# Kernel tuning notes

Hardware: AMD Instinct MI355X
Metric: run time of the kernel (lower is better)

The kernel has to match this reference:

```python
import jax, jax.numpy as jnp
import numpy as np

N = 100000
E = 800000
F_IN = 64
HID = 128


def setup_inputs() -> dict:
    key = jax.random.key(0)
    ks = jax.random.split(key, 10)
    x = jax.random.normal(ks[0], (N, F_IN), dtype=jnp.float32)
    edge_index = jax.random.randint(ks[1], (2, E), 0, N, dtype=jnp.int64)
    s = 0.05
    # PyG GraphConv: lin_rel (with bias) applied to aggregated neighbors, lin_root (no bias) to self
    return {
        "x": x,
        "edge_index": edge_index,
        "W1_rel": jax.random.normal(ks[2], (HID, F_IN), dtype=jnp.float32) * s,
        "b1": jnp.zeros((HID,), dtype=jnp.float32),
        "W1_root": jax.random.normal(ks[3], (HID, F_IN), dtype=jnp.float32) * s,
        "W2_rel": jax.random.normal(ks[4], (HID, HID), dtype=jnp.float32) * s,
        "b2": jnp.zeros((HID,), dtype=jnp.float32),
        "W2_root": jax.random.normal(ks[5], (HID, HID), dtype=jnp.float32) * s,
        "W_fc1": jax.random.normal(ks[6], (20, HID), dtype=jnp.float32) * s,
        "b_fc1": jnp.zeros((20,), dtype=jnp.float32),
        "W_fc2": jax.random.normal(ks[7], (1, 20), dtype=jnp.float32) * s,
        "b_fc2": jnp.zeros((1,), dtype=jnp.float32),
    }


def graph_conv(x, edge_index, W_rel, b_rel, W_root):
    # sum-aggregate source features onto destination nodes (PyG GraphConv, aggr='add')
    src, dst = edge_index[0], edge_index[1]
    agg = jax.ops.segment_sum(x[src], dst, num_segments=N)  # [N, F]
    return agg @ W_rel.T + b_rel + x @ W_root.T


def reference(x, edge_index, W1_rel, b1, W1_root, W2_rel, b2, W2_root,
              W_fc1, b_fc1, W_fc2, b_fc2):
    h = graph_conv(x, edge_index, W1_rel, b1, W1_root)
    h = jax.nn.elu(h)
    h = graph_conv(h, edge_index, W2_rel, b2, W2_root)
    h = jax.nn.relu(h @ W_fc1.T + b_fc1)
    out = h @ W_fc2.T + b_fc2  # [N, 1]
    return out
```

## Files before the change

kernel.cpp:

```cpp
#include <hip/hip_runtime.h>

#define N_NODES 100000
#define N_EDGES 800000
#define FIN 64
#define HID 128
#define NB1 391
#define SRCS_CAP (N_EDGES + 3 * N_NODES)
#define GI (1024 * 256)

typedef unsigned short ushort_t;
typedef __attribute__((ext_vector_type(8))) short short8;
typedef __attribute__((ext_vector_type(16))) float fx16;
typedef __attribute__((ext_vector_type(4))) unsigned short us4;

__device__ inline ushort_t f2bf(float f) {
    unsigned u = __float_as_uint(f);
    u += 0x7fffu + ((u >> 16) & 1u);
    return (ushort_t)(u >> 16);
}

__device__ inline void upadd(float* acc, uint4 A) {
    acc[0] += __uint_as_float(A.x << 16);
    acc[1] += __uint_as_float(A.x & 0xffff0000u);
    acc[2] += __uint_as_float(A.y << 16);
    acc[3] += __uint_as_float(A.y & 0xffff0000u);
    acc[4] += __uint_as_float(A.z << 16);
    acc[5] += __uint_as_float(A.z & 0xffff0000u);
    acc[6] += __uint_as_float(A.w << 16);
    acc[7] += __uint_as_float(A.w & 0xffff0000u);
}

__global__ __launch_bounds__(256) void init_kernel(
    const int* __restrict__ ei, const float* __restrict__ x,
    const float* __restrict__ W1rel, const float* __restrict__ W1root,
    const float* __restrict__ W2rel, const float* __restrict__ W2root,
    int* __restrict__ deg, int* __restrict__ flag, int* __restrict__ srcs,
    ushort_t* __restrict__ xb, ushort_t* __restrict__ h1b,
    ushort_t* __restrict__ Wb1, ushort_t* __restrict__ Wb2) {
    __shared__ int s[256];
    int t = threadIdx.x;
    int gtid = blockIdx.x * 256 + t;

    if (gtid < N_NODES) deg[gtid] = 0;
    for (int k = gtid; k < SRCS_CAP; k += GI) srcs[k] = N_NODES;
    for (int i = gtid; i < N_NODES * FIN / 4; i += GI) {
        float4 v = ((const float4*)x)[i];
        us4 o = {f2bf(v.x), f2bf(v.y), f2bf(v.z), f2bf(v.w)};
        ((us4*)xb)[i] = o;
    }
    us4 z = {0, 0, 0, 0};
    if (gtid < 16) ((us4*)xb)[(size_t)N_NODES * 16 + gtid] = z;
    if (gtid >= 16 && gtid < 48) ((us4*)h1b)[(size_t)N_NODES * 32 + (gtid - 16)] = z;
    if (gtid < HID * HID) {
        int n = gtid >> 7, k = gtid & 127;
        float v = (k < FIN) ? W1rel[n * FIN + k] : W1root[n * FIN + (k - FIN)];
        Wb1[gtid] = f2bf(v);
    }
    if (gtid < HID * 2 * HID) {
        int n = gtid >> 8, k = gtid & 255;
        float v = (k < HID) ? W2rel[n * HID + k] : W2root[n * HID + (k - HID)];
        Wb2[gtid] = f2bf(v);
    }
    if (blockIdx.x == 0) {
        int bad = 0;
        for (int i = t; i < 8192; i += 256) bad |= ei[2 * i + 1];
        s[t] = bad;
        __syncthreads();
        for (int d = 128; d > 0; d >>= 1) {
            if (t < d) s[t] |= s[t + d];
            __syncthreads();
        }
        if (t == 0) *flag = (s[0] != 0) ? 1 : 0;
    }
}

__global__ void hist_kernel(const int* __restrict__ w, const int* __restrict__ flag,
                            int* __restrict__ deg, int* __restrict__ rank) {
    int e = blockIdx.x * 256 + threadIdx.x;
    if (e >= N_EDGES) return;
    int is32 = *flag;
    int d = is32 ? w[N_EDGES + e] : w[2 * (N_EDGES + e)];
    rank[e] = atomicAdd(&deg[d], 1);
}

__global__ void scan1_kernel(const int* __restrict__ deg, int* __restrict__ off,
                             int* __restrict__ bsums) {
    __shared__ int s[256];
    int t = threadIdx.x;
    int i = blockIdx.x * 256 + t;
    int v = (i < N_NODES) ? ((deg[i] + 3) & ~3) : 0;
    s[t] = v;
    __syncthreads();
    for (int d = 1; d < 256; d <<= 1) {
        int w = (t >= d) ? s[t - d] : 0;
        __syncthreads();
        s[t] += w;
        __syncthreads();
    }
    if (i < N_NODES) off[i] = s[t] - v;
    if (t == 255) bsums[blockIdx.x] = s[255];
}

__global__ void scan23_kernel(int* __restrict__ off, const int* __restrict__ bsums) {
    __shared__ int s[256];
    int t = threadIdx.x, b = blockIdx.x;
    int pre = 0, tot = 0;
    for (int j = t; j < NB1; j += 256) {
        int v = bsums[j];
        if (j < b) pre += v;
        tot += v;
    }
    s[t] = pre;
    __syncthreads();
    for (int d = 128; d > 0; d >>= 1) {
        if (t < d) s[t] += s[t + d];
        __syncthreads();
    }
    int prefix = s[0];
    __syncthreads();
    int i = b * 256 + t;
    if (i < N_NODES) off[i] += prefix;
    if (b == 0) {
        s[t] = tot;
        __syncthreads();
        for (int d = 128; d > 0; d >>= 1) {
            if (t < d) s[t] += s[t + d];
            __syncthreads();
        }
        if (t == 0) off[N_NODES] = s[0];
    }
}

__global__ void scatter_kernel(const int* __restrict__ w, const int* __restrict__ flag,
                               const int* __restrict__ off, const int* __restrict__ rank,
                               int* __restrict__ srcs) {
    int e = blockIdx.x * 256 + threadIdx.x;
    if (e >= N_EDGES) return;
    int is32 = *flag;
    int s = is32 ? w[e] : w[2 * e];
    int d = is32 ? w[N_EDGES + e] : w[2 * (N_EDGES + e)];
    srcs[off[d] + rank[e]] = s;
}

__global__ void agg1_kernel(const ushort_t* __restrict__ xb, const int* __restrict__ off,
                            const int* __restrict__ srcs, ushort_t* __restrict__ aggb) {
    int wid = (blockIdx.x * 256 + threadIdx.x) >> 6;
    int lane = threadIdx.x & 63;
    int n = lane >> 3;
    unsigned c = lane & 7;
    int node = wid * 8 + n;
    int b = off[node], e = off[node + 1];
    float acc[8];
#pragma unroll
    for (int j = 0; j < 8; j++) acc[j] = 0.f;
    const uint4* rows = (const uint4*)xb;
    for (int p = b; p < e; p += 4) {
        int4 s = *(const int4*)(srcs + p);
        uint4 A = rows[(unsigned)s.x * 8u + c];
        uint4 B = rows[(unsigned)s.y * 8u + c];
        uint4 C = rows[(unsigned)s.z * 8u + c];
        uint4 D = rows[(unsigned)s.w * 8u + c];
        upadd(acc, A);
        upadd(acc, B);
        upadd(acc, C);
        upadd(acc, D);
    }
    uint4 o = {(unsigned)f2bf(acc[0]) | ((unsigned)f2bf(acc[1]) << 16),
               (unsigned)f2bf(acc[2]) | ((unsigned)f2bf(acc[3]) << 16),
               (unsigned)f2bf(acc[4]) | ((unsigned)f2bf(acc[5]) << 16),
               (unsigned)f2bf(acc[6]) | ((unsigned)f2bf(acc[7]) << 16)};
    ((uint4*)(aggb + (size_t)node * FIN))[c] = o;
}

__global__ void agg2_kernel(const ushort_t* __restrict__ h1b, const int* __restrict__ off,
                            const int* __restrict__ srcs, ushort_t* __restrict__ aggb) {
    int wid = (blockIdx.x * 256 + threadIdx.x) >> 6;
    int lane = threadIdx.x & 63;
    int n = lane >> 4;
    unsigned c = lane & 15;
    int node = wid * 4 + n;
    int b = off[node], e = off[node + 1];
    float acc[8];
#pragma unroll
    for (int j = 0; j < 8; j++) acc[j] = 0.f;
    const uint4* rows = (const uint4*)h1b;
    for (int p = b; p < e; p += 4) {
        int4 s = *(const int4*)(srcs + p);
        uint4 A = rows[(unsigned)s.x * 16u + c];
        uint4 B = rows[(unsigned)s.y * 16u + c];
        uint4 C = rows[(unsigned)s.z * 16u + c];
        uint4 D = rows[(unsigned)s.w * 16u + c];
        upadd(acc, A);
        upadd(acc, B);
        upadd(acc, C);
        upadd(acc, D);
    }
    uint4 o = {(unsigned)f2bf(acc[0]) | ((unsigned)f2bf(acc[1]) << 16),
               (unsigned)f2bf(acc[2]) | ((unsigned)f2bf(acc[3]) << 16),
               (unsigned)f2bf(acc[4]) | ((unsigned)f2bf(acc[5]) << 16),
               (unsigned)f2bf(acc[6]) | ((unsigned)f2bf(acc[7]) << 16)};
    ((uint4*)(aggb + (size_t)node * HID))[c] = o;
}

__global__ __launch_bounds__(256) void g1_kernel(
    const ushort_t* __restrict__ aggb, const ushort_t* __restrict__ xb,
    const ushort_t* __restrict__ Wb1, const float* __restrict__ b1,
    ushort_t* __restrict__ h1b) {
    __shared__ short8 wl8[2048];
    ushort_t* wl = (ushort_t*)wl8;
#pragma unroll
    for (int it = 0; it < 8; it++) {
        int q = it * 256 + threadIdx.x;
        int n = q >> 4, c = q & 15;
        short8 v = ((const short8*)Wb1)[q];
        *(short8*)(wl + n * HID + ((c ^ (n & 7)) << 3)) = v;
    }
    __syncthreads();

    int wave = threadIdx.x >> 6;
    int lane = threadIdx.x & 63;
    int nb = blockIdx.x * 128 + wave * 32;
    if (nb >= N_NODES) return;
    int half = lane >> 5, col = lane & 31;
    int nA = nb + col;
    if (nA >= N_NODES) nA = N_NODES - 1;

    short8 areg[8];
#pragma unroll
    for (int s = 0; s < 4; s++)
        areg[s] = *(const short8*)(aggb + (size_t)nA * FIN + s * 16 + half * 8);
#pragma unroll
    for (int s = 4; s < 8; s++)
        areg[s] = *(const short8*)(xb + (size_t)nA * FIN + (s - 4) * 16 + half * 8);

    fx16 acc[4];
#pragma unroll
    for (int jt = 0; jt < 4; jt++)
#pragma unroll
        for (int r = 0; r < 16; r++) acc[jt][r] = 0.f;

#pragma unroll
    for (int s = 0; s < 8; s++) {
        int c = 2 * s + half;
#pragma unroll
        for (int jt = 0; jt < 4; jt++) {
            int n = jt * 32 + col;
            short8 bq = *(const short8*)(wl + n * HID + ((c ^ (n & 7)) << 3));
            acc[jt] = __builtin_amdgcn_mfma_f32_32x32x16_bf16(areg[s], bq, acc[jt], 0, 0, 0);
        }
    }
#pragma unroll
    for (int jt = 0; jt < 4; jt++) {
        int j = jt * 32 + col;
        float bias = b1[j];
#pragma unroll
        for (int r = 0; r < 16; r++) {
            int node = nb + (r & 3) + 8 * (r >> 2) + 4 * half;
            if (node < N_NODES) {
                float v = acc[jt][r] + bias;
                v = v > 0.f ? v : __expf(v) - 1.f;
                h1b[(size_t)node * HID + j] = f2bf(v);
            }
        }
    }
}

__global__ __launch_bounds__(256) void g2h_kernel(
    const ushort_t* __restrict__ agg2b, const ushort_t* __restrict__ h1b,
    const ushort_t* __restrict__ Wb2, const float* __restrict__ b2,
    const float* __restrict__ Wfc1, const float* __restrict__ bfc1,
    const float* __restrict__ Wfc2, const float* __restrict__ bfc2,
    float* __restrict__ out) {
    __shared__ ushort_t smem[21504];
    ushort_t* wl = smem;
    ushort_t* wf = smem + 17408;

#pragma unroll
    for (int it = 0; it < 16; it++) {
        int idx = it * 256 + threadIdx.x;
        int m = idx >> 7, k = idx & 127;
        float v = (m < 20) ? Wfc1[m * HID + k] : 0.f;
        wf[m * 128 + (((k >> 3) ^ (m & 7)) << 3) + (k & 7)] = f2bf(v);
    }
#pragma unroll
    for (int it = 0; it < 8; it++) {
        int q = it * 256 + threadIdx.x;
        int n = q >> 4, c = q & 15;
        short8 v = *(const short8*)(Wb2 + (size_t)n * 256 + c * 8);
        *(short8*)(wl + n * 128 + ((c ^ (n & 7)) << 3)) = v;
    }

    int wave = threadIdx.x >> 6;
    int lane = threadIdx.x & 63;
    int half = lane >> 5, col = lane & 31;
    int nb = blockIdx.x * 128 + wave * 32;
    int nA = nb + col;
    if (nA >= N_NODES) nA = N_NODES - 1;

    short8 areg[16];
#pragma unroll
    for (int s = 0; s < 8; s++)
        areg[s] = *(const short8*)(agg2b + (size_t)nA * HID + s * 16 + half * 8);
#pragma unroll
    for (int s = 8; s < 16; s++)
        areg[s] = *(const short8*)(h1b + (size_t)nA * HID + (s - 8) * 16 + half * 8);

    fx16 acc[4];
#pragma unroll
    for (int jt = 0; jt < 4; jt++)
#pragma unroll
        for (int r = 0; r < 16; r++) acc[jt][r] = 0.f;

    __syncthreads();
#pragma unroll
    for (int s = 0; s < 8; s++) {
        int c = 2 * s + half;
#pragma unroll
        for (int jt = 0; jt < 4; jt++) {
            int n = jt * 32 + col;
            short8 bq = *(const short8*)(wl + n * 128 + ((c ^ (n & 7)) << 3));
            acc[jt] = __builtin_amdgcn_mfma_f32_32x32x16_bf16(areg[s], bq, acc[jt], 0, 0, 0);
        }
    }
    __syncthreads();
#pragma unroll
    for (int it = 0; it < 8; it++) {
        int q = it * 256 + threadIdx.x;
        int n = q >> 4, c = q & 15;
        short8 v = *(const short8*)(Wb2 + (size_t)n * 256 + 128 + c * 8);
        *(short8*)(wl + n * 128 + ((c ^ (n & 7)) << 3)) = v;
    }
    __syncthreads();
#pragma unroll
    for (int s = 8; s < 16; s++) {
        int c = 2 * (s - 8) + half;
#pragma unroll
        for (int jt = 0; jt < 4; jt++) {
            int n = jt * 32 + col;
            short8 bq = *(const short8*)(wl + n * 128 + ((c ^ (n & 7)) << 3));
            acc[jt] = __builtin_amdgcn_mfma_f32_32x32x16_bf16(areg[s], bq, acc[jt], 0, 0, 0);
        }
    }
    __syncthreads();

    ushort_t* tl = smem;
#pragma unroll
    for (int jt = 0; jt < 4; jt++) {
        int j = jt * 32 + col;
        float bias = b2[j];
#pragma unroll
        for (int r = 0; r < 16; r++) {
            int nl = wave * 32 + (r & 3) + 8 * (r >> 2) + 4 * half;
            tl[nl * 136 + j] = f2bf(acc[jt][r] + bias);
        }
    }
    __syncthreads();

    short8 af[8];
#pragma unroll
    for (int s = 0; s < 8; s++)
        af[s] = *(const short8*)(tl + (wave * 32 + col) * 136 + s * 16 + half * 8);
    fx16 fa;
#pragma unroll
    for (int r = 0; r < 16; r++) fa[r] = 0.f;
#pragma unroll
    for (int s = 0; s < 8; s++) {
        int c = 2 * s + half;
        short8 bw = *(const short8*)(wf + col * 128 + ((c ^ (col & 7)) << 3));
        fa = __builtin_amdgcn_mfma_f32_32x32x16_bf16(af[s], bw, fa, 0, 0, 0);
    }
    float biasv = (col < 20) ? bfc1[col] : 0.f;
    float w2v = (col < 20) ? Wfc2[col] : 0.f;
    float bz = bfc2[0];
    float red[16];
#pragma unroll
    for (int r = 0; r < 16; r++) {
        float v = fa[r] + biasv;
        v = (v > 0.f ? v : 0.f) * w2v;
        v += __shfl_xor(v, 1);
        v += __shfl_xor(v, 2);
        v += __shfl_xor(v, 4);
        v += __shfl_xor(v, 8);
        v += __shfl_xor(v, 16);
        red[r] = v;
    }
    if (col == 0) {
#pragma unroll
        for (int r = 0; r < 16; r++) {
            int nl = wave * 32 + (r & 3) + 8 * (r >> 2) + 4 * half;
            int ng = blockIdx.x * 128 + nl;
            if (ng < N_NODES) out[ng] = red[r] + bz;
        }
    }
}

extern "C" void kernel_launch(void* const* d_in, const int* in_sizes, int n_in,
                              void* d_out, int out_size, void* d_ws, size_t ws_size,
                              hipStream_t stream) {
    const float* x = (const float*)d_in[0];
    const int* ei = (const int*)d_in[1];
    const float* W1rel = (const float*)d_in[2];
    const float* b1 = (const float*)d_in[3];
    const float* W1root = (const float*)d_in[4];
    const float* W2rel = (const float*)d_in[5];
    const float* b2 = (const float*)d_in[6];
    const float* W2root = (const float*)d_in[7];
    const float* Wfc1 = (const float*)d_in[8];
    const float* bfc1 = (const float*)d_in[9];
    const float* Wfc2 = (const float*)d_in[10];
    const float* bfc2 = (const float*)d_in[11];
    float* out = (float*)d_out;

    char* ws = (char*)d_ws;
    size_t o = 0;
    auto alloc = [&](size_t bytes) {
        char* p = ws + o;
        o += (bytes + 255) & ~(size_t)255;
        return p;
    };
    int* deg = (int*)alloc((size_t)N_NODES * 4);
    int* off = (int*)alloc((size_t)(N_NODES + 1) * 4);
    int* bsums = (int*)alloc(4096);
    int* flag = (int*)alloc(256);
    int* rank = (int*)alloc((size_t)N_EDGES * 4);
    int* srcs = (int*)alloc((size_t)SRCS_CAP * 4);
    ushort_t* xb = (ushort_t*)alloc((size_t)(N_NODES + 1) * FIN * 2);
    ushort_t* agg1b = (ushort_t*)alloc((size_t)N_NODES * FIN * 2);
    ushort_t* h1b = (ushort_t*)alloc((size_t)(N_NODES + 1) * HID * 2);
    ushort_t* agg2b = (ushort_t*)alloc((size_t)N_NODES * HID * 2);
    ushort_t* Wb1 = (ushort_t*)alloc((size_t)HID * HID * 2);
    ushort_t* Wb2 = (ushort_t*)alloc((size_t)HID * 2 * HID * 2);

    const int GW = (N_NODES + 127) / 128;
    const int GA1 = N_NODES / 32;
    const int GA2 = N_NODES / 16;

    init_kernel<<<1024, 256, 0, stream>>>(ei, x, W1rel, W1root, W2rel, W2root,
                                          deg, flag, srcs, xb, h1b, Wb1, Wb2);
    hist_kernel<<<(N_EDGES + 255) / 256, 256, 0, stream>>>(ei, flag, deg, rank);
    scan1_kernel<<<NB1, 256, 0, stream>>>(deg, off, bsums);
    scan23_kernel<<<NB1, 256, 0, stream>>>(off, bsums);
    scatter_kernel<<<(N_EDGES + 255) / 256, 256, 0, stream>>>(ei, flag, off, rank, srcs);
    agg1_kernel<<<GA1, 256, 0, stream>>>(xb, off, srcs, agg1b);
    g1_kernel<<<GW, 256, 0, stream>>>(agg1b, xb, Wb1, b1, h1b);
    agg2_kernel<<<GA2, 256, 0, stream>>>(h1b, off, srcs, agg2b);
    g2h_kernel<<<GW, 256, 0, stream>>>(agg2b, h1b, Wb2, b2, Wfc1, bfc1, Wfc2, bfc2, out);
}
```

Baseline: 249.8 us.

## Fold layer-2 weights into fc1 and aggregate projected 20-dim features

```diff
diff --git a/kernel.cpp b/kernel.cpp
--- a/kernel.cpp
+++ b/kernel.cpp
@@ -34,9 +34,11 @@
     const int* __restrict__ ei, const float* __restrict__ x,
     const float* __restrict__ W1rel, const float* __restrict__ W1root,
     const float* __restrict__ W2rel, const float* __restrict__ W2root,
+    const float* __restrict__ b2, const float* __restrict__ Wfc1,
+    const float* __restrict__ bfc1, const float* __restrict__ Wfc2,
     int* __restrict__ deg, int* __restrict__ flag, int* __restrict__ srcs,
-    ushort_t* __restrict__ xb, ushort_t* __restrict__ h1b,
-    ushort_t* __restrict__ Wb1, ushort_t* __restrict__ Wb2) {
+    ushort_t* __restrict__ xb, ushort_t* __restrict__ Wb1,
+    ushort_t* __restrict__ Mb, float* __restrict__ cbp, float* __restrict__ w2p) {
     __shared__ int s[256];
     int t = threadIdx.x;
     int gtid = blockIdx.x * 256 + t;
@@ -50,18 +52,34 @@
     }
     us4 z = {0, 0, 0, 0};
     if (gtid < 16) ((us4*)xb)[(size_t)N_NODES * 16 + gtid] = z;
-    if (gtid >= 16 && gtid < 48) ((us4*)h1b)[(size_t)N_NODES * 32 + (gtid - 16)] = z;
     if (gtid < HID * HID) {
         int n = gtid >> 7, k = gtid & 127;
         float v = (k < FIN) ? W1rel[n * FIN + k] : W1root[n * FIN + (k - FIN)];
         Wb1[gtid] = f2bf(v);
     }
-    if (gtid < HID * 2 * HID) {
-        int n = gtid >> 8, k = gtid & 255;
-        float v = (k < HID) ? W2rel[n * HID + k] : W2root[n * HID + (k - HID)];
-        Wb2[gtid] = f2bf(v);
-    }
-    if (blockIdx.x == 0) {
+    if (blockIdx.x < 32) {
+        int idx = blockIdx.x * 256 + t;
+        int n = idx >> 7, k = idx & 127;
+        float acc = 0.f;
+        if (n < 20) {
+            for (int j = 0; j < HID; j++) acc += Wfc1[n * HID + j] * W2rel[j * HID + k];
+        } else if (n >= 32 && n < 52) {
+            int m = n - 32;
+            for (int j = 0; j < HID; j++) acc += Wfc1[m * HID + j] * W2root[j * HID + k];
+        }
+        Mb[idx] = f2bf(acc);
+    }
+    if (blockIdx.x == 32 && t < 32) {
+        float cv = 0.f, wv = 0.f;
+        if (t < 20) {
+            for (int j = 0; j < HID; j++) cv += Wfc1[t * HID + j] * b2[j];
+            cv += bfc1[t];
+            wv = Wfc2[t];
+        }
+        cbp[t] = cv;
+        w2p[t] = wv;
+    }
+    if (blockIdx.x == 33) {
         int bad = 0;
         for (int i = t; i < 8192; i += 256) bad |= ei[2 * i + 1];
         s[t] = bad;
@@ -172,36 +190,6 @@
     ((uint4*)(aggb + (size_t)node * FIN))[c] = o;
 }
 
-__global__ void agg2_kernel(const ushort_t* __restrict__ h1b, const int* __restrict__ off,
-                            const int* __restrict__ srcs, ushort_t* __restrict__ aggb) {
-    int wid = (blockIdx.x * 256 + threadIdx.x) >> 6;
-    int lane = threadIdx.x & 63;
-    int n = lane >> 4;
-    unsigned c = lane & 15;
-    int node = wid * 4 + n;
-    int b = off[node], e = off[node + 1];
-    float acc[8];
-#pragma unroll
-    for (int j = 0; j < 8; j++) acc[j] = 0.f;
-    const uint4* rows = (const uint4*)h1b;
-    for (int p = b; p < e; p += 4) {
-        int4 s = *(const int4*)(srcs + p);
-        uint4 A = rows[(unsigned)s.x * 16u + c];
-        uint4 B = rows[(unsigned)s.y * 16u + c];
-        uint4 C = rows[(unsigned)s.z * 16u + c];
-        uint4 D = rows[(unsigned)s.w * 16u + c];
-        upadd(acc, A);
-        upadd(acc, B);
-        upadd(acc, C);
-        upadd(acc, D);
-    }
-    uint4 o = {(unsigned)f2bf(acc[0]) | ((unsigned)f2bf(acc[1]) << 16),
-               (unsigned)f2bf(acc[2]) | ((unsigned)f2bf(acc[3]) << 16),
-               (unsigned)f2bf(acc[4]) | ((unsigned)f2bf(acc[5]) << 16),
-               (unsigned)f2bf(acc[6]) | ((unsigned)f2bf(acc[7]) << 16)};
-    ((uint4*)(aggb + (size_t)node * HID))[c] = o;
-}
-
 __global__ __launch_bounds__(256) void g1_kernel(
     const ushort_t* __restrict__ aggb, const ushort_t* __restrict__ xb,
     const ushort_t* __restrict__ Wb1, const float* __restrict__ b1,
@@ -265,133 +253,115 @@
     }
 }
 
-__global__ __launch_bounds__(256) void g2h_kernel(
-    const ushort_t* __restrict__ agg2b, const ushort_t* __restrict__ h1b,
-    const ushort_t* __restrict__ Wb2, const float* __restrict__ b2,
-    const float* __restrict__ Wfc1, const float* __restrict__ bfc1,
-    const float* __restrict__ Wfc2, const float* __restrict__ bfc2,
-    float* __restrict__ out) {
-    __shared__ ushort_t smem[21504];
-    ushort_t* wl = smem;
-    ushort_t* wf = smem + 17408;
-
-#pragma unroll
-    for (int it = 0; it < 16; it++) {
-        int idx = it * 256 + threadIdx.x;
-        int m = idx >> 7, k = idx & 127;
-        float v = (m < 20) ? Wfc1[m * HID + k] : 0.f;
-        wf[m * 128 + (((k >> 3) ^ (m & 7)) << 3) + (k & 7)] = f2bf(v);
-    }
-#pragma unroll
-    for (int it = 0; it < 8; it++) {
+__global__ __launch_bounds__(256) void g2_kernel(
+    const ushort_t* __restrict__ h1b, const ushort_t* __restrict__ Mb,
+    ushort_t* __restrict__ uvb) {
+    __shared__ short8 ml8[1024];
+    ushort_t* ml = (ushort_t*)ml8;
+    us4 z = {0, 0, 0, 0};
+    if (blockIdx.x == 0 && threadIdx.x < 8)
+        ((us4*)(uvb + (size_t)N_NODES * 64))[threadIdx.x] = z;
+#pragma unroll
+    for (int it = 0; it < 4; it++) {
         int q = it * 256 + threadIdx.x;
         int n = q >> 4, c = q & 15;
-        short8 v = *(const short8*)(Wb2 + (size_t)n * 256 + c * 8);
-        *(short8*)(wl + n * 128 + ((c ^ (n & 7)) << 3)) = v;
-    }
+        short8 v = ((const short8*)Mb)[q];
+        *(short8*)(ml + n * HID + ((c ^ (n & 7)) << 3)) = v;
+    }
+    __syncthreads();
 
     int wave = threadIdx.x >> 6;
     int lane = threadIdx.x & 63;
+    int nb = blockIdx.x * 128 + wave * 32;
+    if (nb >= N_NODES) return;
     int half = lane >> 5, col = lane & 31;
-    int nb = blockIdx.x * 128 + wave * 32;
     int nA = nb + col;
     if (nA >= N_NODES) nA = N_NODES - 1;
 
-    short8 areg[16];
+    short8 areg[8];
 #pragma unroll
     for (int s = 0; s < 8; s++)
-        areg[s] = *(const short8*)(agg2b + (size_t)nA * HID + s * 16 + half * 8);
-#pragma unroll
-    for (int s = 8; s < 16; s++)
-        areg[s] = *(const short8*)(h1b + (size_t)nA * HID + (s - 8) * 16 + half * 8);
-
-    fx16 acc[4];
-#pragma unroll
-    for (int jt = 0; jt < 4; jt++)
+        areg[s] = *(const short8*)(h1b + (size_t)nA * HID + s * 16 + half * 8);
+
+    fx16 acc[2];
+#pragma unroll
+    for (int jt = 0; jt < 2; jt++)
 #pragma unroll
         for (int r = 0; r < 16; r++) acc[jt][r] = 0.f;
 
-    __syncthreads();
 #pragma unroll
     for (int s = 0; s < 8; s++) {
         int c = 2 * s + half;
 #pragma unroll
-        for (int jt = 0; jt < 4; jt++) {
+        for (int jt = 0; jt < 2; jt++) {
             int n = jt * 32 + col;
-            short8 bq = *(const short8*)(wl + n * 128 + ((c ^ (n & 7)) << 3));
+            short8 bq = *(const short8*)(ml + n * HID + ((c ^ (n & 7)) << 3));
             acc[jt] = __builtin_amdgcn_mfma_f32_32x32x16_bf16(areg[s], bq, acc[jt], 0, 0, 0);
         }
     }
-    __syncthreads();
-#pragma unroll
-    for (int it = 0; it < 8; it++) {
-        int q = it * 256 + threadIdx.x;
-        int n = q >> 4, c = q & 15;
-        short8 v = *(const short8*)(Wb2 + (size_t)n * 256 + 128 + c * 8);
-        *(short8*)(wl + n * 128 + ((c ^ (n & 7)) << 3)) = v;
-    }
-    __syncthreads();
-#pragma unroll
-    for (int s = 8; s < 16; s++) {
-        int c = 2 * (s - 8) + half;
-#pragma unroll
-        for (int jt = 0; jt < 4; jt++) {
-            int n = jt * 32 + col;
-            short8 bq = *(const short8*)(wl + n * 128 + ((c ^ (n & 7)) << 3));
-            acc[jt] = __builtin_amdgcn_mfma_f32_32x32x16_bf16(areg[s], bq, acc[jt], 0, 0, 0);
-        }
-    }
-    __syncthreads();
-
-    ushort_t* tl = smem;
-#pragma unroll
-    for (int jt = 0; jt < 4; jt++) {
+#pragma unroll
+    for (int jt = 0; jt < 2; jt++) {
         int j = jt * 32 + col;
-        float bias = b2[j];
 #pragma unroll
         for (int r = 0; r < 16; r++) {
-            int nl = wave * 32 + (r & 3) + 8 * (r >> 2) + 4 * half;
-            tl[nl * 136 + j] = f2bf(acc[jt][r] + bias);
-        }
-    }
-    __syncthreads();
-
-    short8 af[8];
-#pragma unroll
-    for (int s = 0; s < 8; s++)
-        af[s] = *(const short8*)(tl + (wave * 32 + col) * 136 + s * 16 + half * 8);
-    fx16 fa;
-#pragma unroll
-    for (int r = 0; r < 16; r++) fa[r] = 0.f;
-#pragma unroll
-    for (int s = 0; s < 8; s++) {
-        int c = 2 * s + half;
-        short8 bw = *(const short8*)(wf + col * 128 + ((c ^ (col & 7)) << 3));
-        fa = __builtin_amdgcn_mfma_f32_32x32x16_bf16(af[s], bw, fa, 0, 0, 0);
-    }
-    float biasv = (col < 20) ? bfc1[col] : 0.f;
-    float w2v = (col < 20) ? Wfc2[col] : 0.f;
-    float bz = bfc2[0];
-    float red[16];
-#pragma unroll
-    for (int r = 0; r < 16; r++) {
-        float v = fa[r] + biasv;
-        v = (v > 0.f ? v : 0.f) * w2v;
-        v += __shfl_xor(v, 1);
-        v += __shfl_xor(v, 2);
-        v += __shfl_xor(v, 4);
-        v += __shfl_xor(v, 8);
-        v += __shfl_xor(v, 16);
-        red[r] = v;
-    }
-    if (col == 0) {
-#pragma unroll
-        for (int r = 0; r < 16; r++) {
-            int nl = wave * 32 + (r & 3) + 8 * (r >> 2) + 4 * half;
-            int ng = blockIdx.x * 128 + nl;
-            if (ng < N_NODES) out[ng] = red[r] + bz;
-        }
-    }
+            int node = nb + (r & 3) + 8 * (r >> 2) + 4 * half;
+            if (node < N_NODES) uvb[(size_t)node * 64 + j] = f2bf(acc[jt][r]);
+        }
+    }
+}
+
+__global__ void agg3h_kernel(const ushort_t* __restrict__ uvb, const int* __restrict__ off,
+                             const int* __restrict__ srcs, const float* __restrict__ cbp,
+                             const float* __restrict__ w2p, const float* __restrict__ bfc2,
+                             float* __restrict__ out) {
+    int wid = (blockIdx.x * 256 + threadIdx.x) >> 6;
+    int lane = threadIdx.x & 63;
+    int n = lane >> 2;
+    unsigned c = lane & 3;
+    int node0 = wid * 16 + n;
+    int node = (node0 < N_NODES) ? node0 : N_NODES - 1;
+    int b = off[node], e = off[node + 1];
+    float acc[8];
+#pragma unroll
+    for (int j = 0; j < 8; j++) acc[j] = 0.f;
+    const uint4* rows = (const uint4*)uvb;
+    for (int p = b; p < e; p += 4) {
+        int4 s = *(const int4*)(srcs + p);
+        uint4 A = rows[(unsigned)s.x * 8u + c];
+        uint4 B = rows[(unsigned)s.y * 8u + c];
+        uint4 C = rows[(unsigned)s.z * 8u + c];
+        uint4 D = rows[(unsigned)s.w * 8u + c];
+        upadd(acc, A);
+        upadd(acc, B);
+        upadd(acc, C);
+        upadd(acc, D);
+    }
+    uint4 V = rows[(size_t)node * 8u + 4u + c];
+    float vv[8];
+    vv[0] = __uint_as_float(V.x << 16);
+    vv[1] = __uint_as_float(V.x & 0xffff0000u);
+    vv[2] = __uint_as_float(V.y << 16);
+    vv[3] = __uint_as_float(V.y & 0xffff0000u);
+    vv[4] = __uint_as_float(V.z << 16);
+    vv[5] = __uint_as_float(V.z & 0xffff0000u);
+    vv[6] = __uint_as_float(V.w << 16);
+    vv[7] = __uint_as_float(V.w & 0xffff0000u);
+    float4 cba = ((const float4*)cbp)[c * 2];
+    float4 cbb = ((const float4*)cbp)[c * 2 + 1];
+    float4 w2a = ((const float4*)w2p)[c * 2];
+    float4 w2b = ((const float4*)w2p)[c * 2 + 1];
+    float s = 0.f, a;
+    a = acc[0] + vv[0] + cba.x; s += (a > 0.f ? a : 0.f) * w2a.x;
+    a = acc[1] + vv[1] + cba.y; s += (a > 0.f ? a : 0.f) * w2a.y;
+    a = acc[2] + vv[2] + cba.z; s += (a > 0.f ? a : 0.f) * w2a.z;
+    a = acc[3] + vv[3] + cba.w; s += (a > 0.f ? a : 0.f) * w2a.w;
+    a = acc[4] + vv[4] + cbb.x; s += (a > 0.f ? a : 0.f) * w2b.x;
+    a = acc[5] + vv[5] + cbb.y; s += (a > 0.f ? a : 0.f) * w2b.y;
+    a = acc[6] + vv[6] + cbb.z; s += (a > 0.f ? a : 0.f) * w2b.z;
+    a = acc[7] + vv[7] + cbb.w; s += (a > 0.f ? a : 0.f) * w2b.w;
+    s += __shfl_xor(s, 1);
+    s += __shfl_xor(s, 2);
+    if (c == 0 && node0 < N_NODES) out[node0] = s + bfc2[0];
 }
 
 extern "C" void kernel_launch(void* const* d_in, const int* in_sizes, int n_in,
@@ -426,23 +396,26 @@
     int* srcs = (int*)alloc((size_t)SRCS_CAP * 4);
     ushort_t* xb = (ushort_t*)alloc((size_t)(N_NODES + 1) * FIN * 2);
     ushort_t* agg1b = (ushort_t*)alloc((size_t)N_NODES * FIN * 2);
-    ushort_t* h1b = (ushort_t*)alloc((size_t)(N_NODES + 1) * HID * 2);
-    ushort_t* agg2b = (ushort_t*)alloc((size_t)N_NODES * HID * 2);
+    ushort_t* h1b = (ushort_t*)alloc((size_t)N_NODES * HID * 2);
+    ushort_t* uvb = (ushort_t*)alloc((size_t)(N_NODES + 1) * 64 * 2);
     ushort_t* Wb1 = (ushort_t*)alloc((size_t)HID * HID * 2);
-    ushort_t* Wb2 = (ushort_t*)alloc((size_t)HID * 2 * HID * 2);
+    ushort_t* Mb = (ushort_t*)alloc((size_t)64 * HID * 2);
+    float* cbp = (float*)alloc(32 * 4);
+    float* w2p = (float*)alloc(32 * 4);
 
     const int GW = (N_NODES + 127) / 128;
     const int GA1 = N_NODES / 32;
-    const int GA2 = N_NODES / 16;
+    const int GA3 = 1563;
 
     init_kernel<<<1024, 256, 0, stream>>>(ei, x, W1rel, W1root, W2rel, W2root,
-                                          deg, flag, srcs, xb, h1b, Wb1, Wb2);
+                                          b2, Wfc1, bfc1, Wfc2,
+                                          deg, flag, srcs, xb, Wb1, Mb, cbp, w2p);
     hist_kernel<<<(N_EDGES + 255) / 256, 256, 0, stream>>>(ei, flag, deg, rank);
     scan1_kernel<<<NB1, 256, 0, stream>>>(deg, off, bsums);
     scan23_kernel<<<NB1, 256, 0, stream>>>(off, bsums);
     scatter_kernel<<<(N_EDGES + 255) / 256, 256, 0, stream>>>(ei, flag, off, rank, srcs);
     agg1_kernel<<<GA1, 256, 0, stream>>>(xb, off, srcs, agg1b);
     g1_kernel<<<GW, 256, 0, stream>>>(agg1b, xb, Wb1, b1, h1b);
-    agg2_kernel<<<GA2, 256, 0, stream>>>(h1b, off, srcs, agg2b);
-    g2h_kernel<<<GW, 256, 0, stream>>>(agg2b, h1b, Wb2, b2, Wfc1, bfc1, Wfc2, bfc2, out);
-}
+    g2_kernel<<<GW, 256, 0, stream>>>(h1b, Mb, uvb);
+    agg3h_kernel<<<GA3, 256, 0, stream>>>(uvb, off, srcs, cbp, w2p, bfc2, out);
+}
```

Measured after the change: 216.1 us. -13.5%, faster.
